# Kernel optimization log

Hardware: AMD Instinct MI355X
Metric: run time of the kernel (lower is better)

The kernel has to match this reference:

```python
import jax, jax.numpy as jnp
import numpy as np

EPS = 1e-8
LN_EPS = 1e-5
MA_K = 25


def _moving_avg(x, k):
    # x: [B, L]; replicate-pad by (k-1)//2 on each side, then length-k mean -> [B, L]
    p = (k - 1) // 2
    xp = jnp.concatenate([jnp.repeat(x[:, :1], p, axis=1), x, jnp.repeat(x[:, -1:], p, axis=1)], axis=1)
    cs = jnp.concatenate([jnp.zeros((x.shape[0], 1), x.dtype), jnp.cumsum(xp, axis=1)], axis=1)
    return (cs[:, k:] - cs[:, :-k]) / k


def _acf(xc, den, lag):
    # xc: mean-centered x [B, L]; den: sum(xc^2)+eps [B]
    num = (xc[:, :-lag] * xc[:, lag:]).sum(axis=1)
    return jnp.clip(num / den, -1.0, 1.0)


def _forward(x, ln_w, ln_b, w1, b1, w2, b2):
    B, L = x.shape
    trend = _moving_avg(x, MA_K)
    resid = x - trend

    m = x.mean(axis=1, keepdims=True)
    xc = x - m
    den = (xc * xc).sum(axis=1) + EPS

    acf1 = _acf(xc, den, 1)
    acf2 = _acf(xc, den, 2)

    # spectral entropy + peak psd ratio (single rfft)
    Xf = jnp.fft.rfft(x, axis=1)
    psd = jnp.maximum(Xf.real ** 2 + Xf.imag ** 2, EPS)
    psd_sum = psd.sum(axis=1)
    psd_n = psd / psd_sum[:, None]
    ent = -(psd_n * jnp.log(psd_n + EPS)).sum(axis=1)
    max_ent = jnp.log(jnp.asarray(psd.shape[1], x.dtype) + EPS)
    spent = jnp.clip(ent / (max_ent + EPS), 0.0, 1.0)
    peak_ratio = jnp.clip(psd.max(axis=1) / (psd_sum + EPS), 0.0, 1.0)

    # unit-root phi
    x_t, x_tm1 = x[:, 1:], x[:, :-1]
    phi = jnp.clip((x_t * x_tm1).sum(axis=1) / ((x_tm1 ** 2).sum(axis=1) + EPS), -1.0, 1.0)

    diff = x_t - x_tm1
    diff_var = jnp.var(diff, axis=1)
    trend_strength = jnp.var(trend, axis=1)
    kpss_proxy = jnp.var(jnp.cumsum(resid, axis=1), axis=1) / (jnp.var(x, axis=1) + 1e-8)

    h = max(1, min(10, L // 4))
    lbq = sum(_acf(xc, den, k) ** 2 for k in range(1, h + 1))

    feats = jnp.stack([acf1, acf2, spent, phi, diff_var, trend_strength, kpss_proxy, lbq, peak_ratio], axis=1)

    # LayerNorm over 9 features
    fm = feats.mean(axis=-1, keepdims=True)
    fv = jnp.var(feats, axis=-1, keepdims=True)
    feats_n = (feats - fm) / jnp.sqrt(fv + LN_EPS) * ln_w + ln_b

    # MLP router: 9 -> 64 -> 3 (dropout=0, temperature=1)
    hdd = jax.nn.relu(feats_n @ w1 + b1)
    logits = hdd @ w2 + b2
    weights = jax.nn.softmax(logits, axis=-1)
    return weights, feats_n


def setup_inputs() -> dict:
    key = jax.random.key(0)
    ks = jax.random.split(key, 5)
    B, L, D, H, C = 32768, 1024, 9, 64, 3
    return {
        "x_n_target": jax.random.normal(ks[0], (B, L), dtype=jnp.float32),
        "ln_w": jnp.ones((D,), jnp.float32),
        "ln_b": jnp.zeros((D,), jnp.float32),
        "w1": jax.random.normal(ks[1], (D, H), dtype=jnp.float32) * 0.3,
        "b1": jnp.zeros((H,), jnp.float32),
        "w2": jax.random.normal(ks[2], (H, C), dtype=jnp.float32) * 0.1,
        "b2": jnp.zeros((C,), jnp.float32),
    }


def reference(x_n_target, ln_w, ln_b, w1, b1, w2, b2):
    return _forward(x_n_target, ln_w, ln_b, w1, b1, w2, b2)
```

## Files before the change

kernel.cpp:

```cpp
#include <hip/hip_runtime.h>
#include <math.h>

#define EPSF 1e-8f

__device__ __forceinline__ float bcf(int x){ return __builtin_bit_cast(float, x); }
__device__ __forceinline__ int   bci(float x){ return __builtin_bit_cast(int, x); }

template<int CTRL, int RM>
__device__ __forceinline__ float dpp0(float v){
  return bcf(__builtin_amdgcn_update_dpp(0, bci(v), CTRL, RM, 0xF, false));
}
__device__ __forceinline__ float rl(float v, int l){
  return bcf(__builtin_amdgcn_readlane(bci(v), l));
}
__device__ __forceinline__ float wave_iscan_add(float v){
  v += dpp0<0x111,0xF>(v);
  v += dpp0<0x112,0xF>(v);
  v += dpp0<0x114,0xF>(v);
  v += dpp0<0x118,0xF>(v);
  v += dpp0<0x142,0xA>(v);
  v += dpp0<0x143,0xC>(v);
  return v;
}
__device__ __forceinline__ float wave_red_add(float v){ return wave_iscan_add(v); }
__device__ __forceinline__ float wave_red_max_pos(float v){
  v = fmaxf(v, dpp0<0x111,0xF>(v));
  v = fmaxf(v, dpp0<0x112,0xF>(v));
  v = fmaxf(v, dpp0<0x114,0xF>(v));
  v = fmaxf(v, dpp0<0x118,0xF>(v));
  v = fmaxf(v, dpp0<0x142,0xA>(v));
  v = fmaxf(v, dpp0<0x143,0xC>(v));
  return v;
}

__device__ __forceinline__ int FL(int i){ return i ^ ((i >> 4) & 15); }

__device__ __forceinline__ void dft8(float* ar, float* ai){
  constexpr float C = 0.70710678118654752f;
  const float t0r=ar[0]+ar[4], t0i=ai[0]+ai[4];
  const float t1r=ar[0]-ar[4], t1i=ai[0]-ai[4];
  const float t2r=ar[2]+ar[6], t2i=ai[2]+ai[6];
  const float t3r=ar[2]-ar[6], t3i=ai[2]-ai[6];
  const float E0r=t0r+t2r, E0i=t0i+t2i;
  const float E1r=t1r+t3i, E1i=t1i-t3r;
  const float E2r=t0r-t2r, E2i=t0i-t2i;
  const float E3r=t1r-t3i, E3i=t1i+t3r;
  const float u0r=ar[1]+ar[5], u0i=ai[1]+ai[5];
  const float u1r=ar[1]-ar[5], u1i=ai[1]-ai[5];
  const float u2r=ar[3]+ar[7], u2i=ai[3]+ai[7];
  const float u3r=ar[3]-ar[7], u3i=ai[3]-ai[7];
  const float O0r=u0r+u2r, O0i=u0i+u2i;
  const float O1r=u1r+u3i, O1i=u1i-u3r;
  const float O2r=u0r-u2r, O2i=u0i-u2i;
  const float O3r=u1r-u3i, O3i=u1i+u3r;
  const float w1r =  C*(O1r+O1i), w1i = C*(O1i-O1r);
  const float w2r =  O2i,         w2i = -O2r;
  const float w3r =  C*(O3i-O3r), w3i = -C*(O3r+O3i);
  ar[0]=E0r+O0r; ai[0]=E0i+O0i;
  ar[4]=E0r-O0r; ai[4]=E0i-O0i;
  ar[1]=E1r+w1r; ai[1]=E1i+w1i;
  ar[5]=E1r-w1r; ai[5]=E1i-w1i;
  ar[2]=E2r+w2r; ai[2]=E2i+w2i;
  ar[6]=E2r-w2r; ai[6]=E2i-w2i;
  ar[3]=E3r+w3r; ai[3]=E3i+w3i;
  ar[7]=E3r-w3r; ai[7]=E3i-w3i;
}

__global__ void __launch_bounds__(128, 2)
sr_kernel(const float* __restrict__ x,
          const float* __restrict__ ln_w, const float* __restrict__ ln_b,
          const float* __restrict__ w1, const float* __restrict__ b1,
          const float* __restrict__ w2, const float* __restrict__ b2,
          float* __restrict__ out, int B)
{
  __shared__ __align__(16) float2 buf2[2][512];
  __shared__ __align__(16) float stats2[2][40];

  const int tid = threadIdx.x;
  const int t   = tid & 63;
  const int wv  = tid >> 6;
  const int row = blockIdx.x * 2 + wv;
  if (row >= B) return;
  const float* __restrict__ xr = x + (size_t)row * 1024;
  float2* buf = buf2[wv];
  float*  st  = stats2[wv];

  const int c0 = t * 16;
  float vv[28];
  {
    const float4 a0 = *reinterpret_cast<const float4*>(xr + c0);
    const float4 a1 = *reinterpret_cast<const float4*>(xr + c0 + 4);
    const float4 a2 = *reinterpret_cast<const float4*>(xr + c0 + 8);
    const float4 a3 = *reinterpret_cast<const float4*>(xr + c0 + 12);
    vv[0]=a0.x; vv[1]=a0.y; vv[2]=a0.z; vv[3]=a0.w;
    vv[4]=a1.x; vv[5]=a1.y; vv[6]=a1.z; vv[7]=a1.w;
    vv[8]=a2.x; vv[9]=a2.y; vv[10]=a2.z; vv[11]=a2.w;
    vv[12]=a3.x; vv[13]=a3.y; vv[14]=a3.z; vv[15]=a3.w;
    if (t < 63) {
      const float4 n0 = *reinterpret_cast<const float4*>(xr + c0 + 16);
      const float4 n1 = *reinterpret_cast<const float4*>(xr + c0 + 20);
      const float4 n2 = *reinterpret_cast<const float4*>(xr + c0 + 24);
      vv[16]=n0.x; vv[17]=n0.y; vv[18]=n0.z; vv[19]=n0.w;
      vv[20]=n1.x; vv[21]=n1.y; vv[22]=n1.z; vv[23]=n1.w;
      vv[24]=n2.x; vv[25]=n2.y; vv[26]=n2.z; vv[27]=n2.w;
    } else {
#pragma unroll
      for (int j = 16; j < 28; ++j) vv[j] = 0.f;
    }
  }
  float pv[12];
  if (t > 0) {
    const float4 p0 = *reinterpret_cast<const float4*>(xr + c0 - 12);
    const float4 p1 = *reinterpret_cast<const float4*>(xr + c0 - 8);
    const float4 p2 = *reinterpret_cast<const float4*>(xr + c0 - 4);
    pv[0]=p0.x; pv[1]=p0.y; pv[2]=p0.z; pv[3]=p0.w;
    pv[4]=p1.x; pv[5]=p1.y; pv[6]=p1.z; pv[7]=p1.w;
    pv[8]=p2.x; pv[9]=p2.y; pv[10]=p2.z; pv[11]=p2.w;
  } else {
#pragma unroll
    for (int j = 0; j < 12; ++j) pv[j] = 0.f;
  }

#pragma unroll
  for (int j = 0; j < 8; ++j)
    buf[FL(8*t + j)] = make_float2(vv[2*j], vv[2*j+1]);

  float zr[8], zi[8];
#pragma unroll
  for (int p = 0; p < 8; ++p) {
    const float2 v = buf[FL(t + 64*p)];
    zr[p] = v.x; zi[p] = v.y;
  }

  {
    float sumsq = 0.f, alt = 0.f;
#pragma unroll
    for (int j = 0; j < 16; ++j) {
      sumsq = fmaf(vv[j], vv[j], sumsq);
      alt += (j & 1) ? -vv[j] : vv[j];
    }
    float r;
    r = wave_red_add(sumsq); if (t == 63) st[0] = r;
    r = wave_red_add(alt);   if (t == 63) st[1] = r;
  }
#pragma unroll
  for (int k = 1; k <= 10; ++k) {
    float acc = 0.f;
#pragma unroll
    for (int j = 0; j < 16; ++j) acc = fmaf(vv[j], vv[j+k], acc);
    float r = wave_red_add(acc);
    if (t == 63) st[1 + k] = r;
  }

  float s[16];
  s[0] = vv[0];
#pragma unroll
  for (int j = 1; j < 16; ++j) s[j] = s[j-1] + vv[j];
  const float cs16 = s[15];
  const float incl = wave_iscan_add(cs16);
  const float excl = incl - cs16;
#pragma unroll
  for (int j = 0; j < 16; ++j) s[j] += excl;
  if (t == 63) st[16] = incl;
  if (t == 0) {
#pragma unroll
    for (int q = 0; q < 10; ++q) st[17 + q] = s[q];
    st[37] = vv[0];
  }
  if (t == 63) {
#pragma unroll
    for (int q = 0; q < 10; ++q) st[27 + q] = s[5 + q];
    st[38] = vv[15];
  }

  float trv[16];
  float str = 0.f, str2 = 0.f;
  {
    float wsum = 0.f;
#pragma unroll
    for (int j = 0; j < 12; ++j) wsum += pv[j];
#pragma unroll
    for (int j = 0; j <= 12; ++j) wsum += vv[j];
#pragma unroll
    for (int jj = 0; jj < 16; ++jj) {
      if (jj > 0) {
        const float addv = vv[jj + 12];
        const float subv = (jj < 13) ? pv[jj - 1] : vv[jj - 13];
        wsum += addv - subv;
      }
      float swc = wsum;
      if (t == 0  && jj < 12) swc += (float)(12 - jj) * vv[0];
      if (t == 63 && jj >= 4) swc += (float)(jj - 3) * vv[15];
      const float tv = swc * 0.04f;
      trv[jj] = tv;
      str += tv;
      str2 = fmaf(tv, tv, str2);
    }
  }
  const float tincl = wave_iscan_add(str);
  if (t == 63) st[12] = tincl;
  { float r = wave_red_add(str2); if (t == 63) st[13] = r; }
  {
    const float texcl = tincl - str;
    float run = texcl, sc = 0.f, sc2 = 0.f;
#pragma unroll
    for (int jj = 0; jj < 16; ++jj) {
      run += trv[jj];
      const float cv = s[jj] - run;
      sc += cv;
      sc2 = fmaf(cv, cv, sc2);
    }
    float r;
    r = wave_red_add(sc);  if (t == 63) st[14] = r;
    r = wave_red_add(sc2); if (t == 63) st[15] = r;
  }

  dft8(zr, zi);
  {
    const float a1 = -0.012271846303085130f * (float)t;
    const float c1 = __cosf(a1), s1 = __sinf(a1);
    const float c2=c1*c1-s1*s1, s2=2.f*c1*s1;
    const float c3=c2*c1-s2*s1, s3=s2*c1+c2*s1;
    const float c4=c2*c2-s2*s2, s4=2.f*c2*s2;
    const float c5=c4*c1-s4*s1, s5=s4*c1+c4*s1;
    const float c6=c3*c3-s3*s3, s6=2.f*c3*s3;
    const float c7=c6*c1-s6*s1, s7=s6*c1+c6*s1;
    const float cq[8] = {1.f,c1,c2,c3,c4,c5,c6,c7};
    const float sq[8] = {0.f,s1,s2,s3,s4,s5,s6,s7};
#pragma unroll
    for (int q = 1; q < 8; ++q) {
      const float r0 = zr[q]*cq[q] - zi[q]*sq[q];
      zi[q] = zr[q]*sq[q] + zi[q]*cq[q];
      zr[q] = r0;
    }
  }
#pragma unroll
  for (int q = 0; q < 8; ++q)
    buf[FL(q*64 + t)] = make_float2(zr[q], zi[q]);
  const int qq = t >> 3;
  const int dd = t & 7;
  const int qb = qq << 6;
#pragma unroll
  for (int e = 0; e < 8; ++e) {
    const float2 z = buf[FL(qb + dd + 8*e)];
    zr[e] = z.x; zi[e] = z.y;
  }
  dft8(zr, zi);
  {
    const float a1 = -0.098174770424681039f * (float)dd;
    const float c1 = __cosf(a1), s1 = __sinf(a1);
    const float c2=c1*c1-s1*s1, s2=2.f*c1*s1;
    const float c3=c2*c1-s2*s1, s3=s2*c1+c2*s1;
    const float c4=c2*c2-s2*s2, s4=2.f*c2*s2;
    const float c5=c4*c1-s4*s1, s5=s4*c1+c4*s1;
    const float c6=c3*c3-s3*s3, s6=2.f*c3*s3;
    const float c7=c6*c1-s6*s1, s7=s6*c1+c6*s1;
    const float cq[8] = {1.f,c1,c2,c3,c4,c5,c6,c7};
    const float sq[8] = {0.f,s1,s2,s3,s4,s5,s6,s7};
#pragma unroll
    for (int q = 1; q < 8; ++q) {
      const float r0 = zr[q]*cq[q] - zi[q]*sq[q];
      zi[q] = zr[q]*sq[q] + zi[q]*cq[q];
      zr[q] = r0;
    }
  }
#pragma unroll
  for (int sA = 0; sA < 8; ++sA)
    buf[FL(qb + sA*8 + dd)] = make_float2(zr[sA], zi[sA]);
#pragma unroll
  for (int d = 0; d < 8; ++d) {
    const float2 z = buf[FL(qb + dd*8 + d)];
    zr[d] = z.x; zi[d] = z.y;
  }
  dft8(zr, zi);

#pragma unroll
  for (int r = 0; r < 8; ++r)
    buf[FL(t*8 + r)] = make_float2(zr[r], zi[r]);
  const int pl = (t == 0) ? 0 : ((t < 8) ? (8 - t) : (71 - t));
  const bool lane0 = (t == 0);
  const float kb = (float)((dd << 3) + qq);
  const float ab = -0.0061359231515425649f * kb;
  const float wbr = __cosf(ab), wbi = __sinf(ab);
  constexpr float RCr[8] = {1.f, 0.98078528040323044f, 0.92387953251128674f, 0.83146961230254524f,
                            0.70710678118654752f, 0.55557023301960222f, 0.38268343236508977f, 0.19509032201612827f};
  constexpr float RCi[8] = {0.f, -0.19509032201612827f, -0.38268343236508977f, -0.55557023301960222f,
                            -0.70710678118654752f, -0.83146961230254524f, -0.92387953251128674f, -0.98078528040323044f};
  float psum = 0.f, pmax = 0.f, plog = 0.f;
#pragma unroll
  for (int r = 0; r < 8; ++r) {
    const int rho = lane0 ? ((8 - r) & 7) : (7 - r);
    const float2 zp = buf[FL(pl*8 + rho)];
    const float Er = 0.5f*(zr[r] + zp.x);
    const float Ei = 0.5f*(zi[r] - zp.y);
    const float Or = 0.5f*(zi[r] + zp.y);
    const float Oi = -0.5f*(zr[r] - zp.x);
    const float wr = wbr*RCr[r] - wbi*RCi[r];
    const float wi = wbr*RCi[r] + wbi*RCr[r];
    const float Xr = Er + wr*Or - wi*Oi;
    const float Xi = Ei + wr*Oi + wi*Or;
    const float pp = fmaxf(Xr*Xr + Xi*Xi, EPSF);
    psum += pp;
    pmax = fmaxf(pmax, pp);
    plog += pp * __logf(pp);
  }
  const float PSUM = rl(wave_red_add(psum), 63);
  const float PMAX = rl(wave_red_max_pos(pmax), 63);
  const float PLOG = rl(wave_red_add(plog), 63);

  const float SUMSQ = st[0];
  const float ALT   = st[1];
  const float STR   = st[12];
  const float STR2  = st[13];
  const float SC    = st[14];
  const float SC2   = st[15];
  const float SUMX  = st[16];
  const float x0    = st[37];
  const float xl    = st[38];

  const float p512b = fmaxf(ALT * ALT, EPSF);
  const float Sr    = PSUM + p512b;
  const float invS  = 1.f / Sr;
  const float PLr   = PLOG + p512b * __logf(p512b);
  const float ent   = __logf(Sr) - PLr * invS;
  const float PMX   = fmaxf(PMAX, p512b);

  const float m = SUMX * (1.f / 1024.f);
  const float den = SUMSQ - 1024.f * m * m + EPSF;
  const float invden = 1.f / den;
  float acf1 = 0.f, acf2 = 0.f, lbq = 0.f, R1v = 0.f;
#pragma unroll
  for (int k = 1; k <= 10; ++k) {
    const float Rkv = st[1 + k];
    const float Slo = st[16 + k];
    const float Shi = st[37 - k];
    const float num = Rkv - m * (Shi + (SUMX - Slo)) + (float)(1024 - k) * m * m;
    const float a = fminf(fmaxf(num * invden, -1.f), 1.f);
    if (k == 1) { acf1 = a; R1v = Rkv; }
    else if (k == 2) acf2 = a;
    lbq += a * a;
  }
  const float spent = fminf(fmaxf(ent / (__logf(513.f + EPSF) + EPSF), 0.f), 1.f);
  const float peak  = fminf(fmaxf(PMX / (Sr + EPSF), 0.f), 1.f);
  const float phi = fminf(fmaxf(R1v / ((SUMSQ - xl * xl) + EPSF), -1.f), 1.f);
  const float invn = 1.f / 1023.f;
  const float sum_d2 = 2.f * SUMSQ - x0 * x0 - xl * xl - 2.f * R1v;
  const float md = (xl - x0) * invn;
  const float diff_var = sum_d2 * invn - md * md;
  const float tstr = STR2 * (1.f / 1024.f) - (STR * (1.f / 1024.f)) * (STR * (1.f / 1024.f));
  const float varx = SUMSQ * (1.f / 1024.f) - m * m;
  const float mc = SC * (1.f / 1024.f);
  const float kpss = (SC2 * (1.f / 1024.f) - mc * mc) / (varx + 1e-8f);

  float f[9] = {acf1, acf2, spent, phi, diff_var, tstr, kpss, lbq, peak};
  float fm = 0.f;
#pragma unroll
  for (int d = 0; d < 9; ++d) fm += f[d];
  fm *= (1.f / 9.f);
  float fv = 0.f;
#pragma unroll
  for (int d = 0; d < 9; ++d) { const float tt = f[d] - fm; fv = fmaf(tt, tt, fv); }
  fv *= (1.f / 9.f);
  const float inl = 1.f / sqrtf(fv + 1e-5f);
  float fn[9];
#pragma unroll
  for (int d = 0; d < 9; ++d) fn[d] = (f[d] - fm) * inl * ln_w[d] + ln_b[d];

  float h = b1[t];
#pragma unroll
  for (int d = 0; d < 9; ++d) h = fmaf(fn[d], w1[d * 64 + t], h);
  h = fmaxf(h, 0.f);
  float l0 = h * w2[t * 3 + 0];
  float l1 = h * w2[t * 3 + 1];
  float l2 = h * w2[t * 3 + 2];
  l0 = wave_red_add(l0);
  l1 = wave_red_add(l1);
  l2 = wave_red_add(l2);
  const float L0 = rl(l0, 63) + b2[0];
  const float L1 = rl(l1, 63) + b2[1];
  const float L2 = rl(l2, 63) + b2[2];
  if (t == 0) {
    const float mx = fmaxf(L0, fmaxf(L1, L2));
    const float e0 = __expf(L0 - mx), e1 = __expf(L1 - mx), e2 = __expf(L2 - mx);
    const float is = 1.f / (e0 + e1 + e2);
    float* o = out + (size_t)row * 3;
    o[0] = e0 * is; o[1] = e1 * is; o[2] = e2 * is;
    float* fo = out + (size_t)B * 3 + (size_t)row * 9;
    fo[0] = fn[0]; fo[1] = fn[1]; fo[2] = fn[2]; fo[3] = fn[3]; fo[4] = fn[4];
    fo[5] = fn[5]; fo[6] = fn[6]; fo[7] = fn[7]; fo[8] = fn[8];
  }
}

extern "C" void kernel_launch(void* const* d_in, const int* in_sizes, int n_in,
                              void* d_out, int out_size, void* d_ws, size_t ws_size,
                              hipStream_t stream) {
  (void)n_in; (void)out_size; (void)d_ws; (void)ws_size;
  const float* x    = (const float*)d_in[0];
  const float* ln_w = (const float*)d_in[1];
  const float* ln_b = (const float*)d_in[2];
  const float* w1   = (const float*)d_in[3];
  const float* b1   = (const float*)d_in[4];
  const float* w2   = (const float*)d_in[5];
  const float* b2   = (const float*)d_in[6];
  float* out = (float*)d_out;
  const int B = in_sizes[0] / 1024;
  sr_kernel<<<(B + 1) / 2, 128, 0, stream>>>(x, ln_w, ln_b, w1, b1, w2, b2, out, B);
}
```

Baseline: 92.45 us.

## Process two rows per wave with packed float2 FFT arithmetic

Each wave now handles two rows. It runs the time-domain statistics for each row in sequence, then interleaves both rows' spectra in LDS so one FFT pass uses 2-wide vector math (packed FP32). The goal is to halve the per-row FFT instruction count and shared-memory round trips by using packed float ops and 16-byte LDS accesses. In exchange the grid shrinks by half, register pressure and LDS size go up, and the row loops are serialized.

```diff
diff --git a/kernel.cpp b/kernel.cpp
--- a/kernel.cpp
+++ b/kernel.cpp
@@ -2,6 +2,8 @@
 #include <math.h>
 
 #define EPSF 1e-8f
+
+typedef float f2v __attribute__((ext_vector_type(2)));
 
 __device__ __forceinline__ float bcf(int x){ return __builtin_bit_cast(float, x); }
 __device__ __forceinline__ int   bci(float x){ return __builtin_bit_cast(int, x); }
@@ -33,29 +35,29 @@
   return v;
 }
 
-__device__ __forceinline__ int FL(int i){ return i ^ ((i >> 4) & 15); }
-
-__device__ __forceinline__ void dft8(float* ar, float* ai){
-  constexpr float C = 0.70710678118654752f;
-  const float t0r=ar[0]+ar[4], t0i=ai[0]+ai[4];
-  const float t1r=ar[0]-ar[4], t1i=ai[0]-ai[4];
-  const float t2r=ar[2]+ar[6], t2i=ai[2]+ai[6];
-  const float t3r=ar[2]-ar[6], t3i=ai[2]-ai[6];
-  const float E0r=t0r+t2r, E0i=t0i+t2i;
-  const float E1r=t1r+t3i, E1i=t1i-t3r;
-  const float E2r=t0r-t2r, E2i=t0i-t2i;
-  const float E3r=t1r-t3i, E3i=t1i+t3r;
-  const float u0r=ar[1]+ar[5], u0i=ai[1]+ai[5];
-  const float u1r=ar[1]-ar[5], u1i=ai[1]-ai[5];
-  const float u2r=ar[3]+ar[7], u2i=ai[3]+ai[7];
-  const float u3r=ar[3]-ar[7], u3i=ai[3]-ai[7];
-  const float O0r=u0r+u2r, O0i=u0i+u2i;
-  const float O1r=u1r+u3i, O1i=u1i-u3r;
-  const float O2r=u0r-u2r, O2i=u0i-u2i;
-  const float O3r=u1r-u3i, O3i=u1i+u3r;
-  const float w1r =  C*(O1r+O1i), w1i = C*(O1i-O1r);
-  const float w2r =  O2i,         w2i = -O2r;
-  const float w3r =  C*(O3i-O3r), w3i = -C*(O3r+O3i);
+__device__ __forceinline__ int FL8(int i){ return i ^ ((i >> 3) & 7); }
+
+__device__ __forceinline__ void dft8p(f2v* ar, f2v* ai){
+  const float C = 0.70710678118654752f;
+  const f2v t0r=ar[0]+ar[4], t0i=ai[0]+ai[4];
+  const f2v t1r=ar[0]-ar[4], t1i=ai[0]-ai[4];
+  const f2v t2r=ar[2]+ar[6], t2i=ai[2]+ai[6];
+  const f2v t3r=ar[2]-ar[6], t3i=ai[2]-ai[6];
+  const f2v E0r=t0r+t2r, E0i=t0i+t2i;
+  const f2v E1r=t1r+t3i, E1i=t1i-t3r;
+  const f2v E2r=t0r-t2r, E2i=t0i-t2i;
+  const f2v E3r=t1r-t3i, E3i=t1i+t3r;
+  const f2v u0r=ar[1]+ar[5], u0i=ai[1]+ai[5];
+  const f2v u1r=ar[1]-ar[5], u1i=ai[1]-ai[5];
+  const f2v u2r=ar[3]+ar[7], u2i=ai[3]+ai[7];
+  const f2v u3r=ar[3]-ar[7], u3i=ai[3]-ai[7];
+  const f2v O0r=u0r+u2r, O0i=u0i+u2i;
+  const f2v O1r=u1r+u3i, O1i=u1i-u3r;
+  const f2v O2r=u0r-u2r, O2i=u0i-u2i;
+  const f2v O3r=u1r-u3i, O3i=u1i+u3r;
+  const f2v w1r =  C*(O1r+O1i), w1i = C*(O1i-O1r);
+  const f2v w2r =  O2i,         w2i = -O2r;
+  const f2v w3r =  C*(O3i-O3r), w3i = -C*(O3r+O3i);
   ar[0]=E0r+O0r; ai[0]=E0i+O0i;
   ar[4]=E0r-O0r; ai[4]=E0i-O0i;
   ar[1]=E1r+w1r; ai[1]=E1i+w1i;
@@ -73,149 +75,156 @@
           const float* __restrict__ w2, const float* __restrict__ b2,
           float* __restrict__ out, int B)
 {
-  __shared__ __align__(16) float2 buf2[2][512];
-  __shared__ __align__(16) float stats2[2][40];
+  __shared__ __align__(16) float bufr2[2][2048];
+  __shared__ __align__(16) float stats2[2][2][40];
 
   const int tid = threadIdx.x;
   const int t   = tid & 63;
   const int wv  = tid >> 6;
-  const int row = blockIdx.x * 2 + wv;
-  if (row >= B) return;
-  const float* __restrict__ xr = x + (size_t)row * 1024;
-  float2* buf = buf2[wv];
-  float*  st  = stats2[wv];
-
-  const int c0 = t * 16;
-  float vv[28];
-  {
-    const float4 a0 = *reinterpret_cast<const float4*>(xr + c0);
-    const float4 a1 = *reinterpret_cast<const float4*>(xr + c0 + 4);
-    const float4 a2 = *reinterpret_cast<const float4*>(xr + c0 + 8);
-    const float4 a3 = *reinterpret_cast<const float4*>(xr + c0 + 12);
-    vv[0]=a0.x; vv[1]=a0.y; vv[2]=a0.z; vv[3]=a0.w;
-    vv[4]=a1.x; vv[5]=a1.y; vv[6]=a1.z; vv[7]=a1.w;
-    vv[8]=a2.x; vv[9]=a2.y; vv[10]=a2.z; vv[11]=a2.w;
-    vv[12]=a3.x; vv[13]=a3.y; vv[14]=a3.z; vv[15]=a3.w;
-    if (t < 63) {
-      const float4 n0 = *reinterpret_cast<const float4*>(xr + c0 + 16);
-      const float4 n1 = *reinterpret_cast<const float4*>(xr + c0 + 20);
-      const float4 n2 = *reinterpret_cast<const float4*>(xr + c0 + 24);
-      vv[16]=n0.x; vv[17]=n0.y; vv[18]=n0.z; vv[19]=n0.w;
-      vv[20]=n1.x; vv[21]=n1.y; vv[22]=n1.z; vv[23]=n1.w;
-      vv[24]=n2.x; vv[25]=n2.y; vv[26]=n2.z; vv[27]=n2.w;
+  const int rowbase = blockIdx.x * 4 + wv * 2;
+  if (rowbase >= B) return;
+  float* buff = bufr2[wv];
+
+#pragma unroll 1
+  for (int rr = 0; rr < 2; ++rr) {
+    const float* __restrict__ xr = x + (size_t)(rowbase + rr) * 1024;
+    float* st = stats2[wv][rr];
+
+    const int c0 = t * 16;
+    float vv[28];
+    {
+      const float4 a0 = *reinterpret_cast<const float4*>(xr + c0);
+      const float4 a1 = *reinterpret_cast<const float4*>(xr + c0 + 4);
+      const float4 a2 = *reinterpret_cast<const float4*>(xr + c0 + 8);
+      const float4 a3 = *reinterpret_cast<const float4*>(xr + c0 + 12);
+      vv[0]=a0.x; vv[1]=a0.y; vv[2]=a0.z; vv[3]=a0.w;
+      vv[4]=a1.x; vv[5]=a1.y; vv[6]=a1.z; vv[7]=a1.w;
+      vv[8]=a2.x; vv[9]=a2.y; vv[10]=a2.z; vv[11]=a2.w;
+      vv[12]=a3.x; vv[13]=a3.y; vv[14]=a3.z; vv[15]=a3.w;
+      if (t < 63) {
+        const float4 n0 = *reinterpret_cast<const float4*>(xr + c0 + 16);
+        const float4 n1 = *reinterpret_cast<const float4*>(xr + c0 + 20);
+        const float4 n2 = *reinterpret_cast<const float4*>(xr + c0 + 24);
+        vv[16]=n0.x; vv[17]=n0.y; vv[18]=n0.z; vv[19]=n0.w;
+        vv[20]=n1.x; vv[21]=n1.y; vv[22]=n1.z; vv[23]=n1.w;
+        vv[24]=n2.x; vv[25]=n2.y; vv[26]=n2.z; vv[27]=n2.w;
+      } else {
+#pragma unroll
+        for (int j = 16; j < 28; ++j) vv[j] = 0.f;
+      }
+    }
+    float pv[12];
+    if (t > 0) {
+      const float4 p0 = *reinterpret_cast<const float4*>(xr + c0 - 12);
+      const float4 p1 = *reinterpret_cast<const float4*>(xr + c0 - 8);
+      const float4 p2 = *reinterpret_cast<const float4*>(xr + c0 - 4);
+      pv[0]=p0.x; pv[1]=p0.y; pv[2]=p0.z; pv[3]=p0.w;
+      pv[4]=p1.x; pv[5]=p1.y; pv[6]=p1.z; pv[7]=p1.w;
+      pv[8]=p2.x; pv[9]=p2.y; pv[10]=p2.z; pv[11]=p2.w;
     } else {
 #pragma unroll
-      for (int j = 16; j < 28; ++j) vv[j] = 0.f;
-    }
-  }
-  float pv[12];
-  if (t > 0) {
-    const float4 p0 = *reinterpret_cast<const float4*>(xr + c0 - 12);
-    const float4 p1 = *reinterpret_cast<const float4*>(xr + c0 - 8);
-    const float4 p2 = *reinterpret_cast<const float4*>(xr + c0 - 4);
-    pv[0]=p0.x; pv[1]=p0.y; pv[2]=p0.z; pv[3]=p0.w;
-    pv[4]=p1.x; pv[5]=p1.y; pv[6]=p1.z; pv[7]=p1.w;
-    pv[8]=p2.x; pv[9]=p2.y; pv[10]=p2.z; pv[11]=p2.w;
-  } else {
-#pragma unroll
-    for (int j = 0; j < 12; ++j) pv[j] = 0.f;
-  }
-
-#pragma unroll
-  for (int j = 0; j < 8; ++j)
-    buf[FL(8*t + j)] = make_float2(vv[2*j], vv[2*j+1]);
-
-  float zr[8], zi[8];
+      for (int j = 0; j < 12; ++j) pv[j] = 0.f;
+    }
+
+#pragma unroll
+    for (int j = 0; j < 8; ++j) {
+      const int fo = FL8(8*t + j) * 4 + rr;
+      buff[fo]     = vv[2*j];
+      buff[fo + 2] = vv[2*j + 1];
+    }
+
+    {
+      float sumsq = 0.f, alt = 0.f;
+#pragma unroll
+      for (int j = 0; j < 16; ++j) {
+        sumsq = fmaf(vv[j], vv[j], sumsq);
+        alt += (j & 1) ? -vv[j] : vv[j];
+      }
+      float r;
+      r = wave_red_add(sumsq); if (t == 63) st[0] = r;
+      r = wave_red_add(alt);   if (t == 63) st[1] = r;
+    }
+#pragma unroll
+    for (int k = 1; k <= 10; ++k) {
+      float acc = 0.f;
+#pragma unroll
+      for (int j = 0; j < 16; ++j) acc = fmaf(vv[j], vv[j+k], acc);
+      float r = wave_red_add(acc);
+      if (t == 63) st[1 + k] = r;
+    }
+
+    float s[16];
+    s[0] = vv[0];
+#pragma unroll
+    for (int j = 1; j < 16; ++j) s[j] = s[j-1] + vv[j];
+    const float cs16 = s[15];
+    const float incl = wave_iscan_add(cs16);
+    const float excl = incl - cs16;
+#pragma unroll
+    for (int j = 0; j < 16; ++j) s[j] += excl;
+    if (t == 63) st[16] = incl;
+    if (t == 0) {
+#pragma unroll
+      for (int q = 0; q < 10; ++q) st[17 + q] = s[q];
+      st[37] = vv[0];
+    }
+    if (t == 63) {
+#pragma unroll
+      for (int q = 0; q < 10; ++q) st[27 + q] = s[5 + q];
+      st[38] = vv[15];
+    }
+
+    float trv[16];
+    float str = 0.f, str2 = 0.f;
+    {
+      float wsum = 0.f;
+#pragma unroll
+      for (int j = 0; j < 12; ++j) wsum += pv[j];
+#pragma unroll
+      for (int j = 0; j <= 12; ++j) wsum += vv[j];
+#pragma unroll
+      for (int jj = 0; jj < 16; ++jj) {
+        if (jj > 0) {
+          const float addv = vv[jj + 12];
+          const float subv = (jj < 13) ? pv[jj - 1] : vv[jj - 13];
+          wsum += addv - subv;
+        }
+        float swc = wsum;
+        if (t == 0  && jj < 12) swc += (float)(12 - jj) * vv[0];
+        if (t == 63 && jj >= 4) swc += (float)(jj - 3) * vv[15];
+        const float tv = swc * 0.04f;
+        trv[jj] = tv;
+        str += tv;
+        str2 = fmaf(tv, tv, str2);
+      }
+    }
+    const float tincl = wave_iscan_add(str);
+    if (t == 63) st[12] = tincl;
+    { float r = wave_red_add(str2); if (t == 63) st[13] = r; }
+    {
+      const float texcl = tincl - str;
+      float run = texcl, sc = 0.f, sc2 = 0.f;
+#pragma unroll
+      for (int jj = 0; jj < 16; ++jj) {
+        run += trv[jj];
+        const float cv = s[jj] - run;
+        sc += cv;
+        sc2 = fmaf(cv, cv, sc2);
+      }
+      float r;
+      r = wave_red_add(sc);  if (t == 63) st[14] = r;
+      r = wave_red_add(sc2); if (t == 63) st[15] = r;
+    }
+  }
+
+  f2v zr[8], zi[8];
 #pragma unroll
   for (int p = 0; p < 8; ++p) {
-    const float2 v = buf[FL(t + 64*p)];
-    zr[p] = v.x; zi[p] = v.y;
-  }
-
-  {
-    float sumsq = 0.f, alt = 0.f;
-#pragma unroll
-    for (int j = 0; j < 16; ++j) {
-      sumsq = fmaf(vv[j], vv[j], sumsq);
-      alt += (j & 1) ? -vv[j] : vv[j];
-    }
-    float r;
-    r = wave_red_add(sumsq); if (t == 63) st[0] = r;
-    r = wave_red_add(alt);   if (t == 63) st[1] = r;
-  }
-#pragma unroll
-  for (int k = 1; k <= 10; ++k) {
-    float acc = 0.f;
-#pragma unroll
-    for (int j = 0; j < 16; ++j) acc = fmaf(vv[j], vv[j+k], acc);
-    float r = wave_red_add(acc);
-    if (t == 63) st[1 + k] = r;
-  }
-
-  float s[16];
-  s[0] = vv[0];
-#pragma unroll
-  for (int j = 1; j < 16; ++j) s[j] = s[j-1] + vv[j];
-  const float cs16 = s[15];
-  const float incl = wave_iscan_add(cs16);
-  const float excl = incl - cs16;
-#pragma unroll
-  for (int j = 0; j < 16; ++j) s[j] += excl;
-  if (t == 63) st[16] = incl;
-  if (t == 0) {
-#pragma unroll
-    for (int q = 0; q < 10; ++q) st[17 + q] = s[q];
-    st[37] = vv[0];
-  }
-  if (t == 63) {
-#pragma unroll
-    for (int q = 0; q < 10; ++q) st[27 + q] = s[5 + q];
-    st[38] = vv[15];
-  }
-
-  float trv[16];
-  float str = 0.f, str2 = 0.f;
-  {
-    float wsum = 0.f;
-#pragma unroll
-    for (int j = 0; j < 12; ++j) wsum += pv[j];
-#pragma unroll
-    for (int j = 0; j <= 12; ++j) wsum += vv[j];
-#pragma unroll
-    for (int jj = 0; jj < 16; ++jj) {
-      if (jj > 0) {
-        const float addv = vv[jj + 12];
-        const float subv = (jj < 13) ? pv[jj - 1] : vv[jj - 13];
-        wsum += addv - subv;
-      }
-      float swc = wsum;
-      if (t == 0  && jj < 12) swc += (float)(12 - jj) * vv[0];
-      if (t == 63 && jj >= 4) swc += (float)(jj - 3) * vv[15];
-      const float tv = swc * 0.04f;
-      trv[jj] = tv;
-      str += tv;
-      str2 = fmaf(tv, tv, str2);
-    }
-  }
-  const float tincl = wave_iscan_add(str);
-  if (t == 63) st[12] = tincl;
-  { float r = wave_red_add(str2); if (t == 63) st[13] = r; }
-  {
-    const float texcl = tincl - str;
-    float run = texcl, sc = 0.f, sc2 = 0.f;
-#pragma unroll
-    for (int jj = 0; jj < 16; ++jj) {
-      run += trv[jj];
-      const float cv = s[jj] - run;
-      sc += cv;
-      sc2 = fmaf(cv, cv, sc2);
-    }
-    float r;
-    r = wave_red_add(sc);  if (t == 63) st[14] = r;
-    r = wave_red_add(sc2); if (t == 63) st[15] = r;
-  }
-
-  dft8(zr, zi);
+    const float4 q4 = *reinterpret_cast<const float4*>(&buff[FL8(t + 64*p) * 4]);
+    zr[p] = f2v{q4.x, q4.y};
+    zi[p] = f2v{q4.z, q4.w};
+  }
+  dft8p(zr, zi);
   {
     const float a1 = -0.012271846303085130f * (float)t;
     const float c1 = __cosf(a1), s1 = __sinf(a1);
@@ -229,23 +238,27 @@
     const float sq[8] = {0.f,s1,s2,s3,s4,s5,s6,s7};
 #pragma unroll
     for (int q = 1; q < 8; ++q) {
-      const float r0 = zr[q]*cq[q] - zi[q]*sq[q];
+      const f2v r0 = zr[q]*cq[q] - zi[q]*sq[q];
       zi[q] = zr[q]*sq[q] + zi[q]*cq[q];
       zr[q] = r0;
     }
   }
 #pragma unroll
-  for (int q = 0; q < 8; ++q)
-    buf[FL(q*64 + t)] = make_float2(zr[q], zi[q]);
+  for (int q = 0; q < 8; ++q) {
+    const int fo = FL8(q*64 + t) * 4;
+    *reinterpret_cast<f2v*>(&buff[fo])     = zr[q];
+    *reinterpret_cast<f2v*>(&buff[fo + 2]) = zi[q];
+  }
   const int qq = t >> 3;
   const int dd = t & 7;
   const int qb = qq << 6;
 #pragma unroll
   for (int e = 0; e < 8; ++e) {
-    const float2 z = buf[FL(qb + dd + 8*e)];
-    zr[e] = z.x; zi[e] = z.y;
-  }
-  dft8(zr, zi);
+    const float4 q4 = *reinterpret_cast<const float4*>(&buff[FL8(qb + dd + 8*e) * 4]);
+    zr[e] = f2v{q4.x, q4.y};
+    zi[e] = f2v{q4.z, q4.w};
+  }
+  dft8p(zr, zi);
   {
     const float a1 = -0.098174770424681039f * (float)dd;
     const float c1 = __cosf(a1), s1 = __sinf(a1);
@@ -259,24 +272,31 @@
     const float sq[8] = {0.f,s1,s2,s3,s4,s5,s6,s7};
 #pragma unroll
     for (int q = 1; q < 8; ++q) {
-      const float r0 = zr[q]*cq[q] - zi[q]*sq[q];
+      const f2v r0 = zr[q]*cq[q] - zi[q]*sq[q];
       zi[q] = zr[q]*sq[q] + zi[q]*cq[q];
       zr[q] = r0;
     }
   }
 #pragma unroll
-  for (int sA = 0; sA < 8; ++sA)
-    buf[FL(qb + sA*8 + dd)] = make_float2(zr[sA], zi[sA]);
+  for (int sA = 0; sA < 8; ++sA) {
+    const int fo = FL8(qb + sA*8 + dd) * 4;
+    *reinterpret_cast<f2v*>(&buff[fo])     = zr[sA];
+    *reinterpret_cast<f2v*>(&buff[fo + 2]) = zi[sA];
+  }
 #pragma unroll
   for (int d = 0; d < 8; ++d) {
-    const float2 z = buf[FL(qb + dd*8 + d)];
-    zr[d] = z.x; zi[d] = z.y;
-  }
-  dft8(zr, zi);
-
-#pragma unroll
-  for (int r = 0; r < 8; ++r)
-    buf[FL(t*8 + r)] = make_float2(zr[r], zi[r]);
+    const float4 q4 = *reinterpret_cast<const float4*>(&buff[FL8(qb + dd*8 + d) * 4]);
+    zr[d] = f2v{q4.x, q4.y};
+    zi[d] = f2v{q4.z, q4.w};
+  }
+  dft8p(zr, zi);
+
+#pragma unroll
+  for (int r = 0; r < 8; ++r) {
+    const int fo = FL8(t*8 + r) * 4;
+    *reinterpret_cast<f2v*>(&buff[fo])     = zr[r];
+    *reinterpret_cast<f2v*>(&buff[fo + 2]) = zi[r];
+  }
   const int pl = (t == 0) ? 0 : ((t < 8) ? (8 - t) : (71 - t));
   const bool lane0 = (t == 0);
   const float kb = (float)((dd << 3) + qq);
@@ -286,108 +306,124 @@
                             0.70710678118654752f, 0.55557023301960222f, 0.38268343236508977f, 0.19509032201612827f};
   constexpr float RCi[8] = {0.f, -0.19509032201612827f, -0.38268343236508977f, -0.55557023301960222f,
                             -0.70710678118654752f, -0.83146961230254524f, -0.92387953251128674f, -0.98078528040323044f};
-  float psum = 0.f, pmax = 0.f, plog = 0.f;
+  float psA = 0.f, psB = 0.f, pmA = 0.f, pmB = 0.f, plA = 0.f, plB = 0.f;
 #pragma unroll
   for (int r = 0; r < 8; ++r) {
     const int rho = lane0 ? ((8 - r) & 7) : (7 - r);
-    const float2 zp = buf[FL(pl*8 + rho)];
-    const float Er = 0.5f*(zr[r] + zp.x);
-    const float Ei = 0.5f*(zi[r] - zp.y);
-    const float Or = 0.5f*(zi[r] + zp.y);
-    const float Oi = -0.5f*(zr[r] - zp.x);
+    const float4 q4 = *reinterpret_cast<const float4*>(&buff[FL8(pl*8 + rho) * 4]);
+    const f2v zpr = f2v{q4.x, q4.y};
+    const f2v zpi = f2v{q4.z, q4.w};
+    const f2v Er = 0.5f*(zr[r] + zpr);
+    const f2v Ei = 0.5f*(zi[r] - zpi);
+    const f2v Or = 0.5f*(zi[r] + zpi);
+    const f2v Oi = -0.5f*(zr[r] - zpr);
     const float wr = wbr*RCr[r] - wbi*RCi[r];
     const float wi = wbr*RCi[r] + wbi*RCr[r];
-    const float Xr = Er + wr*Or - wi*Oi;
-    const float Xi = Ei + wr*Oi + wi*Or;
-    const float pp = fmaxf(Xr*Xr + Xi*Xi, EPSF);
-    psum += pp;
-    pmax = fmaxf(pmax, pp);
-    plog += pp * __logf(pp);
-  }
-  const float PSUM = rl(wave_red_add(psum), 63);
-  const float PMAX = rl(wave_red_max_pos(pmax), 63);
-  const float PLOG = rl(wave_red_add(plog), 63);
-
-  const float SUMSQ = st[0];
-  const float ALT   = st[1];
-  const float STR   = st[12];
-  const float STR2  = st[13];
-  const float SC    = st[14];
-  const float SC2   = st[15];
-  const float SUMX  = st[16];
-  const float x0    = st[37];
-  const float xl    = st[38];
-
-  const float p512b = fmaxf(ALT * ALT, EPSF);
-  const float Sr    = PSUM + p512b;
-  const float invS  = 1.f / Sr;
-  const float PLr   = PLOG + p512b * __logf(p512b);
-  const float ent   = __logf(Sr) - PLr * invS;
-  const float PMX   = fmaxf(PMAX, p512b);
-
-  const float m = SUMX * (1.f / 1024.f);
-  const float den = SUMSQ - 1024.f * m * m + EPSF;
-  const float invden = 1.f / den;
-  float acf1 = 0.f, acf2 = 0.f, lbq = 0.f, R1v = 0.f;
-#pragma unroll
-  for (int k = 1; k <= 10; ++k) {
-    const float Rkv = st[1 + k];
-    const float Slo = st[16 + k];
-    const float Shi = st[37 - k];
-    const float num = Rkv - m * (Shi + (SUMX - Slo)) + (float)(1024 - k) * m * m;
-    const float a = fminf(fmaxf(num * invden, -1.f), 1.f);
-    if (k == 1) { acf1 = a; R1v = Rkv; }
-    else if (k == 2) acf2 = a;
-    lbq += a * a;
-  }
-  const float spent = fminf(fmaxf(ent / (__logf(513.f + EPSF) + EPSF), 0.f), 1.f);
-  const float peak  = fminf(fmaxf(PMX / (Sr + EPSF), 0.f), 1.f);
-  const float phi = fminf(fmaxf(R1v / ((SUMSQ - xl * xl) + EPSF), -1.f), 1.f);
-  const float invn = 1.f / 1023.f;
-  const float sum_d2 = 2.f * SUMSQ - x0 * x0 - xl * xl - 2.f * R1v;
-  const float md = (xl - x0) * invn;
-  const float diff_var = sum_d2 * invn - md * md;
-  const float tstr = STR2 * (1.f / 1024.f) - (STR * (1.f / 1024.f)) * (STR * (1.f / 1024.f));
-  const float varx = SUMSQ * (1.f / 1024.f) - m * m;
-  const float mc = SC * (1.f / 1024.f);
-  const float kpss = (SC2 * (1.f / 1024.f) - mc * mc) / (varx + 1e-8f);
-
-  float f[9] = {acf1, acf2, spent, phi, diff_var, tstr, kpss, lbq, peak};
-  float fm = 0.f;
-#pragma unroll
-  for (int d = 0; d < 9; ++d) fm += f[d];
-  fm *= (1.f / 9.f);
-  float fv = 0.f;
-#pragma unroll
-  for (int d = 0; d < 9; ++d) { const float tt = f[d] - fm; fv = fmaf(tt, tt, fv); }
-  fv *= (1.f / 9.f);
-  const float inl = 1.f / sqrtf(fv + 1e-5f);
-  float fn[9];
-#pragma unroll
-  for (int d = 0; d < 9; ++d) fn[d] = (f[d] - fm) * inl * ln_w[d] + ln_b[d];
-
-  float h = b1[t];
-#pragma unroll
-  for (int d = 0; d < 9; ++d) h = fmaf(fn[d], w1[d * 64 + t], h);
-  h = fmaxf(h, 0.f);
-  float l0 = h * w2[t * 3 + 0];
-  float l1 = h * w2[t * 3 + 1];
-  float l2 = h * w2[t * 3 + 2];
-  l0 = wave_red_add(l0);
-  l1 = wave_red_add(l1);
-  l2 = wave_red_add(l2);
-  const float L0 = rl(l0, 63) + b2[0];
-  const float L1 = rl(l1, 63) + b2[1];
-  const float L2 = rl(l2, 63) + b2[2];
-  if (t == 0) {
-    const float mx = fmaxf(L0, fmaxf(L1, L2));
-    const float e0 = __expf(L0 - mx), e1 = __expf(L1 - mx), e2 = __expf(L2 - mx);
-    const float is = 1.f / (e0 + e1 + e2);
-    float* o = out + (size_t)row * 3;
-    o[0] = e0 * is; o[1] = e1 * is; o[2] = e2 * is;
-    float* fo = out + (size_t)B * 3 + (size_t)row * 9;
-    fo[0] = fn[0]; fo[1] = fn[1]; fo[2] = fn[2]; fo[3] = fn[3]; fo[4] = fn[4];
-    fo[5] = fn[5]; fo[6] = fn[6]; fo[7] = fn[7]; fo[8] = fn[8];
+    const f2v Xr = Er + wr*Or - wi*Oi;
+    const f2v Xi = Ei + wr*Oi + wi*Or;
+    const f2v pp = Xr*Xr + Xi*Xi;
+    const float pa = fmaxf(pp.x, EPSF);
+    const float pb = fmaxf(pp.y, EPSF);
+    psA += pa; psB += pb;
+    pmA = fmaxf(pmA, pa); pmB = fmaxf(pmB, pb);
+    plA += pa * __logf(pa);
+    plB += pb * __logf(pb);
+  }
+  float PSUM2[2], PMAX2[2], PLOG2[2];
+  PSUM2[0] = rl(wave_red_add(psA), 63);
+  PSUM2[1] = rl(wave_red_add(psB), 63);
+  PMAX2[0] = rl(wave_red_max_pos(pmA), 63);
+  PMAX2[1] = rl(wave_red_max_pos(pmB), 63);
+  PLOG2[0] = rl(wave_red_add(plA), 63);
+  PLOG2[1] = rl(wave_red_add(plB), 63);
+
+#pragma unroll 1
+  for (int rr = 0; rr < 2; ++rr) {
+    const float* st = stats2[wv][rr];
+    const int row = rowbase + rr;
+    const float PSUM = PSUM2[rr], PMAX = PMAX2[rr], PLOG = PLOG2[rr];
+
+    const float SUMSQ = st[0];
+    const float ALT   = st[1];
+    const float STR   = st[12];
+    const float STR2  = st[13];
+    const float SC    = st[14];
+    const float SC2   = st[15];
+    const float SUMX  = st[16];
+    const float x0    = st[37];
+    const float xl    = st[38];
+
+    const float p512b = fmaxf(ALT * ALT, EPSF);
+    const float Sr    = PSUM + p512b;
+    const float invS  = 1.f / Sr;
+    const float PLr   = PLOG + p512b * __logf(p512b);
+    const float ent   = __logf(Sr) - PLr * invS;
+    const float PMX   = fmaxf(PMAX, p512b);
+
+    const float m = SUMX * (1.f / 1024.f);
+    const float den = SUMSQ - 1024.f * m * m + EPSF;
+    const float invden = 1.f / den;
+    float acf1 = 0.f, acf2 = 0.f, lbq = 0.f, R1v = 0.f;
+#pragma unroll
+    for (int k = 1; k <= 10; ++k) {
+      const float Rkv = st[1 + k];
+      const float Slo = st[16 + k];
+      const float Shi = st[37 - k];
+      const float num = Rkv - m * (Shi + (SUMX - Slo)) + (float)(1024 - k) * m * m;
+      const float a = fminf(fmaxf(num * invden, -1.f), 1.f);
+      if (k == 1) { acf1 = a; R1v = Rkv; }
+      else if (k == 2) acf2 = a;
+      lbq += a * a;
+    }
+    const float spent = fminf(fmaxf(ent / (__logf(513.f + EPSF) + EPSF), 0.f), 1.f);
+    const float peak  = fminf(fmaxf(PMX / (Sr + EPSF), 0.f), 1.f);
+    const float phi = fminf(fmaxf(R1v / ((SUMSQ - xl * xl) + EPSF), -1.f), 1.f);
+    const float invn = 1.f / 1023.f;
+    const float sum_d2 = 2.f * SUMSQ - x0 * x0 - xl * xl - 2.f * R1v;
+    const float md = (xl - x0) * invn;
+    const float diff_var = sum_d2 * invn - md * md;
+    const float tstr = STR2 * (1.f / 1024.f) - (STR * (1.f / 1024.f)) * (STR * (1.f / 1024.f));
+    const float varx = SUMSQ * (1.f / 1024.f) - m * m;
+    const float mc = SC * (1.f / 1024.f);
+    const float kpss = (SC2 * (1.f / 1024.f) - mc * mc) / (varx + 1e-8f);
+
+    float f[9] = {acf1, acf2, spent, phi, diff_var, tstr, kpss, lbq, peak};
+    float fm = 0.f;
+#pragma unroll
+    for (int d = 0; d < 9; ++d) fm += f[d];
+    fm *= (1.f / 9.f);
+    float fv = 0.f;
+#pragma unroll
+    for (int d = 0; d < 9; ++d) { const float tt = f[d] - fm; fv = fmaf(tt, tt, fv); }
+    fv *= (1.f / 9.f);
+    const float inl = 1.f / sqrtf(fv + 1e-5f);
+    float fn[9];
+#pragma unroll
+    for (int d = 0; d < 9; ++d) fn[d] = (f[d] - fm) * inl * ln_w[d] + ln_b[d];
+
+    float h = b1[t];
+#pragma unroll
+    for (int d = 0; d < 9; ++d) h = fmaf(fn[d], w1[d * 64 + t], h);
+    h = fmaxf(h, 0.f);
+    float l0 = h * w2[t * 3 + 0];
+    float l1 = h * w2[t * 3 + 1];
+    float l2 = h * w2[t * 3 + 2];
+    l0 = wave_red_add(l0);
+    l1 = wave_red_add(l1);
+    l2 = wave_red_add(l2);
+    const float L0 = rl(l0, 63) + b2[0];
+    const float L1 = rl(l1, 63) + b2[1];
+    const float L2 = rl(l2, 63) + b2[2];
+    if (t == 0) {
+      const float mx = fmaxf(L0, fmaxf(L1, L2));
+      const float e0 = __expf(L0 - mx), e1 = __expf(L1 - mx), e2 = __expf(L2 - mx);
+      const float is = 1.f / (e0 + e1 + e2);
+      float* o = out + (size_t)row * 3;
+      o[0] = e0 * is; o[1] = e1 * is; o[2] = e2 * is;
+      float* fo = out + (size_t)B * 3 + (size_t)row * 9;
+      fo[0] = fn[0]; fo[1] = fn[1]; fo[2] = fn[2]; fo[3] = fn[3]; fo[4] = fn[4];
+      fo[5] = fn[5]; fo[6] = fn[6]; fo[7] = fn[7]; fo[8] = fn[8];
+    }
   }
 }
 
@@ -404,5 +440,5 @@
   const float* b2   = (const float*)d_in[6];
   float* out = (float*)d_out;
   const int B = in_sizes[0] / 1024;
-  sr_kernel<<<(B + 1) / 2, 128, 0, stream>>>(x, ln_w, ln_b, w1, b1, w2, b2, out, B);
-}
+  sr_kernel<<<(B + 3) / 4, 128, 0, stream>>>(x, ln_w, ln_b, w1, b1, w2, b2, out, B);
+}
```

New measurement: 82.90 us, median of 2. -10.3%, faster.
